# Kernel optimization log

Measured on AMD Instinct MI355X. Metric: run time of the kernel, lower is better.

The kernel has to match this reference:

```python
import jax, jax.numpy as jnp
import numpy as np

SR = 22050
N_SAMPLES = 131072
N_FRAMES = 256
WS = 2048
STEP = WS // 2
C = 32
K = WS // 2 + 1
N_LAYERS = 3
B = 4
SPF = N_SAMPLES // N_FRAMES  # samples per frame = 512


def _morlet(M, w, s):
    # scipy.signal.morlet (complete=True)
    x = np.linspace(-s * 2 * np.pi, s * 2 * np.pi, M)
    return (np.exp(1j * w * x) - np.exp(-0.5 * w ** 2)) * np.exp(-0.5 * x ** 2) * np.pi ** -0.25


def _make_filter_bank():
    # musical_scale_hz(21, 129, K)
    midi = np.linspace(21.0, 129.0, K)
    hz = 440.0 * 2.0 ** ((midi - 69.0) / 12.0)
    basis = np.zeros((K, WS), dtype=np.complex128)
    s = 0.025
    for i, f in enumerate(hz):
        w = f / (s * 2 * SR / WS)
        basis[i] = _morlet(WS, w, s)
    basis = basis.real
    basis = basis / (np.linalg.norm(basis, axis=-1, keepdims=True) + 1e-8)
    # abs(rfft(fb, norm='ortho'))
    spec = np.abs(np.fft.rfft(basis, axis=-1) / np.sqrt(WS))
    return jnp.asarray(spec, dtype=jnp.float32)  # (K, K)


def _hann():
    # torch.hann_window default is periodic
    return 0.5 - 0.5 * jnp.cos(2.0 * jnp.pi * jnp.arange(WS) / WS)


def _windowed_audio(x):
    # pad right by step, unfold into overlapping frames, apply hann window
    xp = jnp.pad(x, ((0, 0), (0, 0), (0, STEP)))
    nf = (xp.shape[-1] - WS) // STEP + 1  # = 128
    idx = jnp.arange(nf)[:, None] * STEP + jnp.arange(WS)[None, :]
    frames = xp[..., idx]  # (B, C, F, WS)
    return frames * _hann()


def _overlap_add(frames):
    # apply_window=True: hann at synthesis, hop = WS//2
    x = frames * _hann()
    b, c, f, w = x.shape
    hop = w // 2
    first = x[..., :hop].reshape(b, c, f * hop)
    second = x[..., hop:].reshape(b, c, f * hop)
    return jnp.pad(first, ((0, 0), (0, 0), (0, hop))) + jnp.pad(second, ((0, 0), (0, 0), (hop, 0)))


def _fft_convolve(a, b):
    n = a.shape[-1]
    pa = [(0, 0)] * (a.ndim - 1) + [(0, n)]
    pb = [(0, 0)] * (b.ndim - 1) + [(0, n)]
    spec = jnp.fft.rfft(jnp.pad(a, pa), axis=-1) * jnp.fft.rfft(jnp.pad(b, pb), axis=-1)
    return jnp.fft.irfft(spec, axis=-1)[..., :n]


def _block(x, transfer, mixer_mat, gain, filter_bank):
    t = x.shape[-1]
    x = jnp.einsum('bct,cd->bdt', x, mixer_mat)  # channel mixing
    frames = _windowed_audio(x)                  # (B, C, F, WS)
    spec = jnp.fft.rfft(frames, axis=-1)         # (B, C, F, K) complex
    T = (transfer @ filter_bank).astype(spec.dtype)  # (C, K)
    spec_f = jnp.moveaxis(spec, 2, 0)            # (F, B, C, K)
    init = jnp.zeros(spec_f.shape[1:], dtype=spec.dtype)

    def step(carry, s):
        out = (s + carry) * T
        return out, out

    _, outs = jax.lax.scan(step, init, spec_f)   # linear recurrence over frames
    out = jnp.moveaxis(outs, 0, 2)               # (B, C, F, K)
    wins = jnp.fft.irfft(out, axis=-1)           # (B, C, F, WS)
    samples = _overlap_add(wins)
    samples = jnp.tanh(samples * gain[None, :, None])
    return samples[..., :t]


def _network(x, transfers, mixer_mats, gains, mixer, filter_bank):
    outputs = [x]
    inp = x
    for i in range(N_LAYERS):
        inp = _block(inp, transfers[i], mixer_mats[i], gains[i], filter_bank)
        outputs.append(inp)
    result = jnp.stack(outputs, axis=-1)         # (B, C, T, L+1)
    w = jax.nn.softmax(mixer)
    mixed = (result * w).sum(-1)                 # mixture over layer outputs
    return mixed.sum(axis=1, keepdims=True)      # (B, 1, T)


def setup_inputs() -> dict:
    key = jax.random.key(0)
    ks = jax.random.split(key, 8)
    sig = jax.random.uniform(ks[0], (B, C, N_FRAMES), dtype=jnp.float32) * 1e-2
    noise = jax.random.uniform(ks[1], (N_SAMPLES,), minval=-1.0, maxval=1.0, dtype=jnp.float32)
    channel_decays = jax.random.uniform(ks[2], (C,), dtype=jnp.float32)
    mixer = jax.random.normal(ks[3], (N_LAYERS + 1,), dtype=jnp.float32)
    res = jax.random.uniform(ks[4], (N_LAYERS, C, K), minval=0.5, maxval=0.9998, dtype=jnp.float32)
    mask = (jax.random.uniform(ks[5], (N_LAYERS, C, K)) < 0.01).astype(jnp.float32)
    transfers = res * mask                       # sparse resonances (p=0.01)
    mixer_mats = jnp.tile(jnp.eye(C, dtype=jnp.float32)[None], (N_LAYERS, 1, 1))
    gains = jax.random.uniform(ks[6], (N_LAYERS, C), minval=1.0, maxval=50.0, dtype=jnp.float32)
    filter_bank = _make_filter_bank()
    return dict(sig=sig, noise=noise, channel_decays=channel_decays, mixer=mixer,
                transfers=transfers, mixer_mats=mixer_mats, gains=gains, filter_bank=filter_bank)


def reference(sig, noise, channel_decays, mixer, transfers, mixer_mats, gains, filter_bank):
    # upsample_with_holes
    us = jnp.zeros((sig.shape[0], C, N_SAMPLES), dtype=sig.dtype).at[..., ::SPF].set(sig)
    # per-channel decaying envelopes
    ls = jnp.linspace(1.0, 0.0, SPF, dtype=sig.dtype)[None, None, :] ** channel_decays[None, :, None]
    ls = jnp.pad(ls, ((0, 0), (0, 0), (0, N_SAMPLES - SPF)))
    us = _fft_convolve(us, ls) * noise
    result = _network(us, transfers, mixer_mats, gains, mixer, filter_bank)
    return result, sig
```

## Files before the change

### kernel.cpp

```cpp
#include <hip/hip_runtime.h>
#include <math.h>

constexpr int BB   = 4;
constexpr int CC   = 32;
constexpr int TT   = 131072;
constexpr int NFRM = 128;
constexpr int KK   = 1025;
constexpr int HOP  = 1024;
constexpr int SPF  = 512;
constexpr int SIGF = 256;
constexpr int NL   = 3;
constexpr int RST  = 2052;
constexpr int NBC  = BB*CC;
constexpr int NROWS = NBC*NFRM;
constexpr int MAXNZ = 256;
constexpr int GRP  = 8;
constexpr int FPG  = 16;

#define PD4(a) ((a) + ((a) >> 3))

__device__ __forceinline__ float4 f4add(float4 a, float4 b){return make_float4(a.x+b.x,a.y+b.y,a.z+b.z,a.w+b.w);}
__device__ __forceinline__ float4 f4sub(float4 a, float4 b){return make_float4(a.x-b.x,a.y-b.y,a.z-b.z,a.w-b.w);}
__device__ __forceinline__ float4 cmul4(float4 v, float c, float s){
  return make_float4(v.x*c - v.y*s, v.x*s + v.y*c, v.z*c - v.w*s, v.z*s + v.w*c);
}

template<int SGN>
__device__ __forceinline__ void dft4p(float4 v[4]) {
  float4 b0=f4add(v[0],v[2]), b1=f4sub(v[0],v[2]), b2=f4add(v[1],v[3]), b3=f4sub(v[1],v[3]);
  float4 ib3 = (SGN<0)? make_float4(b3.y,-b3.x,b3.w,-b3.z) : make_float4(-b3.y,b3.x,-b3.w,b3.z);
  v[0]=f4add(b0,b2); v[2]=f4sub(b0,b2);
  v[1]=f4add(b1,ib3); v[3]=f4sub(b1,ib3);
}

template<int SGN, bool FINAL_STORE>
__device__ __forceinline__ void stockham_pair(float4 v[4], float4* S4, int tid) {
  #pragma unroll
  for (int Ns=1; Ns<1024; Ns*=4) {
    if (Ns>1) {
      int k = tid & (Ns-1);
      float ang = (float)SGN * 6.28318530717958647692f * (float)k / (float)(4*Ns);
      float s1,c1; __sincosf(ang,&s1,&c1);
      float c2=c1*c1-s1*s1, s2=2.f*c1*s1;
      float c3=c2*c1-s2*s1, s3=c2*s1+s2*c1;
      v[1]=cmul4(v[1],c1,s1); v[2]=cmul4(v[2],c2,s2); v[3]=cmul4(v[3],c3,s3);
    }
    dft4p<SGN>(v);
    if (Ns<256 || FINAL_STORE) {
      int idxD = ((tid & ~(Ns-1))<<2) | (tid & (Ns-1));
      S4[PD4(idxD       )] = v[0];
      S4[PD4(idxD +   Ns)] = v[1];
      S4[PD4(idxD + 2*Ns)] = v[2];
      S4[PD4(idxD + 3*Ns)] = v[3];
      __syncthreads();
      if (Ns<256) {
        v[0]=S4[PD4(tid)]; v[1]=S4[PD4(tid+256)]; v[2]=S4[PD4(tid+512)]; v[3]=S4[PD4(tid+768)];
        __syncthreads();
      }
    }
  }
}

__global__ void k_tables(const float* __restrict__ decay, float* __restrict__ ENVt,
                         float* __restrict__ HANN, float* __restrict__ PKt,
                         float* __restrict__ UPKt) {
  int gid = blockIdx.x*256 + threadIdx.x;
  if (gid < CC*SPF) {
    int c = gid >> 9, r = gid & 511;
    float d = decay[c];
    float env;
    if (r == 511) env = (d == 0.f) ? 1.f : 0.f;
    else          env = powf((float)(511-r)*(1.0f/511.0f), d);
    ENVt[gid] = env;
  }
  if (gid < 2048) HANN[gid] = 0.5f - 0.5f*cosf((float)gid*(float)(M_PI/1024.0));
  if (gid <= 1024) { float s,c; sincosf(-(float)M_PI*(float)gid*(1.0f/1024.0f),&s,&c); PKt[2*gid]=c; PKt[2*gid+1]=s; }
  if (gid <  1024) { float s,c; sincosf( (float)M_PI*(float)gid*(1.0f/1024.0f),&s,&c); UPKt[2*gid]=c; UPKt[2*gid+1]=s; }
}

__global__ void __launch_bounds__(64) k_nnz(const float* __restrict__ tr,
    int* __restrict__ NZI, float* __restrict__ NZV, int* __restrict__ NZC) {
  int lc = blockIdx.x;
  int lane = threadIdx.x;
  const float* trow = tr + (size_t)lc*KK;
  int base = 0;
  for (int start = 0; start < KK; start += 64) {
    int kp = start + lane;
    float v = (kp < KK) ? trow[kp] : 0.f;
    unsigned long long m = __ballot(v != 0.f);
    int pos = base + __popcll(m & ((1ull<<lane)-1ull));
    if (v != 0.f && pos < MAXNZ) { NZI[lc*MAXNZ+pos] = kp; NZV[lc*MAXNZ+pos] = v; }
    base += __popcll(m);
  }
  if (lane == 0) NZC[lc] = (base < MAXNZ) ? base : MAXNZ;
}

__global__ void __launch_bounds__(256) k_tmat2(const int* __restrict__ NZI,
    const float* __restrict__ NZV, const int* __restrict__ NZC,
    const float* __restrict__ fb, float* __restrict__ TM) {
  int gid = blockIdx.x*256 + threadIdx.x;
  if (gid >= NL*CC*KK) return;
  int k = gid % KK, lc = gid / KK;
  int n = NZC[lc];
  const int*   zi = NZI + lc*MAXNZ;
  const float* zv = NZV + lc*MAXNZ;
  float acc = 0.f;
  for (int i = 0; i < n; ++i)
    acc = fmaf(zv[i], fb[(size_t)zi[i]*KK + k], acc);
  TM[gid] = acc;
}

__global__ void k_ident(const float* __restrict__ mats, int* __restrict__ FLG) {
  int l = blockIdx.x;
  const float* M = mats + (size_t)l*CC*CC;
  __shared__ int ok;
  if (threadIdx.x == 0) ok = 1;
  __syncthreads();
  for (int i = threadIdx.x; i < CC*CC; i += 256) {
    float ex = ((i>>5) == (i&31)) ? 1.f : 0.f;
    if (M[i] != ex) ok = 0;
  }
  __syncthreads();
  if (threadIdx.x == 0) FLG[l] = ok;
}

__global__ void __launch_bounds__(256) k_us_init(const float* __restrict__ sig,
    const float* __restrict__ noise, const float* __restrict__ mixer,
    const float* __restrict__ M0, const float* __restrict__ ENVt,
    float* __restrict__ X, float* __restrict__ out) {
  __shared__ float sM[CC*CC];
  int tid = threadIdx.x;
  for (int i = tid; i < CC*CC; i += 256) sM[i] = M0[i];
  __syncthreads();
  int gid = blockIdx.x*256 + tid;
  int b = gid >> 17, t = gid & (TT-1);
  int q = t >> 9, r = t & 511;
  float nz = noise[t];
  float u[CC]; float s = 0.f;
  #pragma unroll
  for (int c = 0; c < CC; ++c) { u[c] = sig[(b*CC+c)*SIGF + q] * ENVt[c*SPF + r]; s += u[c]; }
  float m0=mixer[0],m1=mixer[1],m2=mixer[2],m3=mixer[3];
  float mx=fmaxf(fmaxf(m0,m1),fmaxf(m2,m3));
  float e0=__expf(m0-mx),e1=__expf(m1-mx),e2=__expf(m2-mx),e3=__expf(m3-mx);
  float w0=e0/(e0+e1+e2+e3);
  out[gid] = w0 * nz * s;
  #pragma unroll
  for (int d = 0; d < CC; ++d) {
    float acc = 0.f;
    #pragma unroll
    for (int c = 0; c < CC; ++c) acc = fmaf(u[c], sM[c*CC+d], acc);
    X[(size_t)(b*CC+d)*TT + t] = nz * acc;
  }
  if (gid < BB*CC*SIGF) out[BB*TT + gid] = sig[gid];
}

__global__ void __launch_bounds__(256) k_mix_cond(float* __restrict__ X,
    const float* __restrict__ M, const int* __restrict__ FLG, int layer) {
  if (FLG[layer]) return;
  __shared__ float sM[CC*CC];
  int tid = threadIdx.x;
  for (int i = tid; i < CC*CC; i += 256) sM[i] = M[i];
  __syncthreads();
  int gid = blockIdx.x*256 + tid;
  int b = gid >> 17, t = gid & (TT-1);
  float* xp = X + (size_t)b*CC*TT + t;
  float xv[CC];
  #pragma unroll
  for (int c = 0; c < CC; ++c) xv[c] = xp[(size_t)c*TT];
  for (int d = 0; d < CC; ++d) {
    float acc = 0.f;
    #pragma unroll
    for (int c = 0; c < CC; ++c) acc = fmaf(xv[c], sM[c*CC+d], acc);
    xp[(size_t)d*TT] = acc;
  }
}

__global__ void __launch_bounds__(256) k_fwd_scan(const float* __restrict__ X,
    float* __restrict__ SPEC, float* __restrict__ EB, const float* __restrict__ TM,
    const float* __restrict__ HANN, const float* __restrict__ PKt) {
  __shared__ float4 S4[1152];
  int tid = threadIdx.x;
  int blk = blockIdx.x;
  int g = blk & (GRP-1), bc = blk >> 3;
  int c = bc & (CC-1);
  const float* xr = X + (size_t)bc*TT;
  float Tv[5]; float2 cr[5];
  #pragma unroll
  for (int j = 0; j < 5; ++j) {
    int k = tid + 256*j;
    Tv[j] = (k <= 1024) ? TM[c*KK + k] : 0.f;
    cr[j] = make_float2(0.f, 0.f);
  }
  for (int p = 0; p < 8; ++p) {
    int f0 = g*FPG + 2*p;
    int s0 = f0*HOP;
    float4 v[4];
    #pragma unroll
    for (int r = 0; r < 4; ++r) {
      int n = tid + 256*r;
      float2 h = *(const float2*)(HANN + 2*n);
      float2 a = *(const float2*)(xr + s0 + 2*n);
      int sb = s0 + HOP + 2*n;
      float2 bb = (sb < TT) ? *(const float2*)(xr + sb) : make_float2(0.f,0.f);
      v[r] = make_float4(a.x*h.x, a.y*h.y, bb.x*h.x, bb.y*h.y);
    }
    stockham_pair<-1, true>(v, S4, tid);
    float* row0 = SPEC + (size_t)(bc*NFRM + f0)*RST;
    float* row1 = row0 + RST;
    #pragma unroll
    for (int j = 0; j < 5; ++j) {
      int k = tid + 256*j;
      if (k <= 1024) {
        float4 Zk = S4[PD4(k & 1023)];
        float4 Zm = S4[PD4((1024-k) & 1023)];
        float2 pk = *(const float2*)(PKt + 2*k);
        float zex = 0.5f*(Zk.x+Zm.x), zey = 0.5f*(Zk.y-Zm.y);
        float zox = 0.5f*(Zk.y+Zm.y), zoy = -0.5f*(Zk.x-Zm.x);
        float sax = zex + pk.x*zox - pk.y*zoy;
        float say = zey + pk.x*zoy + pk.y*zox;
        zex = 0.5f*(Zk.z+Zm.z); zey = 0.5f*(Zk.w-Zm.w);
        zox = 0.5f*(Zk.w+Zm.w); zoy = -0.5f*(Zk.z-Zm.z);
        float sbx = zex + pk.x*zox - pk.y*zoy;
        float sby = zey + pk.x*zoy + pk.y*zox;
        cr[j].x = (sax + cr[j].x)*Tv[j];
        cr[j].y = (say + cr[j].y)*Tv[j];
        *(float2*)(row0 + 2*k) = cr[j];
        cr[j].x = (sbx + cr[j].x)*Tv[j];
        cr[j].y = (sby + cr[j].y)*Tv[j];
        *(float2*)(row1 + 2*k) = cr[j];
      }
    }
    __syncthreads();
  }
  float* er = EB + (size_t)blk*RST;
  #pragma unroll
  for (int j = 0; j < 5; ++j) {
    int k = tid + 256*j;
    if (k <= 1024) *(float2*)(er + 2*k) = cr[j];
  }
}

__global__ void __launch_bounds__(256) k_carry(float* __restrict__ EB, const float* __restrict__ TM) {
  int gid = blockIdx.x*256 + threadIdx.x;
  if (gid >= NBC*KK) return;
  int bc = gid / KK, k = gid - bc*KK;
  int c = bc & (CC-1);
  float T = TM[c*KK + k];
  float t2 = T*T, t4 = t2*t2, t8 = t4*t4, T16 = t8*t8;
  float2 cc = make_float2(0.f, 0.f);
  for (int g = 0; g < GRP; ++g) {
    float* p = EB + (size_t)(bc*GRP + g)*RST + 2*k;
    float2 e = *(float2*)p;
    *(float2*)p = cc;
    cc.x = e.x + T16*cc.x;
    cc.y = e.y + T16*cc.y;
  }
}

__global__ void __launch_bounds__(256) k_inv_ola(const float* __restrict__ SPEC,
    const float* __restrict__ EB, const float* __restrict__ TM,
    const float* __restrict__ HANN, const float* __restrict__ UPKt,
    const float* __restrict__ gains, float* __restrict__ X) {
  __shared__ float4 S4[1152];
  int tid = threadIdx.x;
  int blk = blockIdx.x;
  int g = blk & (GRP-1), bc = blk >> 3;
  int c = bc & (CC-1);
  int fb = g*FPG;
  float sg = gains[c];
  const float* ec = EB + (size_t)blk*RST;
  float Tn[4], Tm[4], facn[4], facm[4];
  float2 cinN[4], cinM[4];
  #pragma unroll
  for (int r = 0; r < 4; ++r) {
    int n = tid + 256*r, m = 1024 - n;
    Tn[r] = TM[c*KK + n]; Tm[r] = TM[c*KK + m];
    facn[r] = Tn[r]; facm[r] = Tm[r];
    cinN[r] = *(const float2*)(ec + 2*n);
    cinM[r] = *(const float2*)(ec + 2*m);
  }
  float2 pr0 = make_float2(0.f,0.f), pr1 = make_float2(0.f,0.f);
  float* xw = X + (size_t)bc*TT;
  const float sc = 1.0f/1024.0f;
  for (int rnd = 0; rnd < 9; ++rnd) {
    float4 v[4];
    #pragma unroll
    for (int r = 0; r < 4; ++r) {
      int n = tid + 256*r, m = 1024 - n;
      float2 An, Am, Bn, Bm;
      if (rnd == 0) { An = cinN[r]; Am = cinM[r]; }
      else {
        const float* rowA = SPEC + (size_t)(bc*NFRM + fb + 2*rnd - 1)*RST;
        float2 a = *(const float2*)(rowA + 2*n);
        float2 b = *(const float2*)(rowA + 2*m);
        An = make_float2(a.x + facn[r]*cinN[r].x, a.y + facn[r]*cinN[r].y);
        Am = make_float2(b.x + facm[r]*cinM[r].x, b.y + facm[r]*cinM[r].y);
        facn[r] *= Tn[r]; facm[r] *= Tm[r];
      }
      if (rnd < 8) {
        const float* rowB = SPEC + (size_t)(bc*NFRM + fb + 2*rnd)*RST;
        float2 a = *(const float2*)(rowB + 2*n);
        float2 b = *(const float2*)(rowB + 2*m);
        Bn = make_float2(a.x + facn[r]*cinN[r].x, a.y + facn[r]*cinN[r].y);
        Bm = make_float2(b.x + facm[r]*cinM[r].x, b.y + facm[r]*cinM[r].y);
        facn[r] *= Tn[r]; facm[r] *= Tm[r];
      } else { Bn = make_float2(0.f,0.f); Bm = make_float2(0.f,0.f); }
      float2 u = *(const float2*)(UPKt + 2*n);
      float zex = 0.5f*(An.x+Am.x), zey = 0.5f*(An.y-Am.y);
      float dx  = 0.5f*(An.x-Am.x), dy  = 0.5f*(An.y+Am.y);
      float zox = u.x*dx - u.y*dy, zoy = u.x*dy + u.y*dx;
      v[r].x = zex - zoy; v[r].y = zey + zox;
      zex = 0.5f*(Bn.x+Bm.x); zey = 0.5f*(Bn.y-Bm.y);
      dx  = 0.5f*(Bn.x-Bm.x); dy  = 0.5f*(Bn.y+Bm.y);
      zox = u.x*dx - u.y*dy; zoy = u.x*dy + u.y*dx;
      v[r].z = zex - zoy; v[r].w = zey + zox;
    }
    stockham_pair<1, false>(v, S4, tid);
    #pragma unroll
    for (int r = 0; r < 4; ++r) {
      int n = tid + 256*r;
      float2 h = *(const float2*)(HANN + 2*n);
      v[r].x *= sc*h.x; v[r].y *= sc*h.y;
      v[r].z *= sc*h.x; v[r].w *= sc*h.y;
    }
    if (rnd >= 1) {
      int tbase = (fb + 2*rnd - 1)*HOP;
      float2 o0 = make_float2(tanhf(sg*(v[0].x + pr0.x)), tanhf(sg*(v[0].y + pr0.y)));
      float2 o1 = make_float2(tanhf(sg*(v[1].x + pr1.x)), tanhf(sg*(v[1].y + pr1.y)));
      *(float2*)(xw + tbase + 2*tid)        = o0;
      *(float2*)(xw + tbase + 2*(tid+256))  = o1;
    }
    if (rnd < 8) {
      int tbase = (fb + 2*rnd)*HOP;
      float2 o0 = make_float2(tanhf(sg*(v[0].z + v[2].x)), tanhf(sg*(v[0].w + v[2].y)));
      float2 o1 = make_float2(tanhf(sg*(v[1].z + v[3].x)), tanhf(sg*(v[1].w + v[3].y)));
      *(float2*)(xw + tbase + 2*tid)        = o0;
      *(float2*)(xw + tbase + 2*(tid+256))  = o1;
      pr0 = make_float2(v[2].z, v[2].w);
      pr1 = make_float2(v[3].z, v[3].w);
    }
  }
}

__global__ void __launch_bounds__(256) k_out(const float* __restrict__ X,
    const float* __restrict__ mixer, int layer, float* __restrict__ out) {
  int gid = blockIdx.x*256 + threadIdx.x;
  int t4 = gid*4;
  int b = t4 >> 17, t = t4 & (TT-1);
  float m0=mixer[0],m1=mixer[1],m2=mixer[2],m3=mixer[3];
  float mx=fmaxf(fmaxf(m0,m1),fmaxf(m2,m3));
  float e[4]={__expf(m0-mx),__expf(m1-mx),__expf(m2-mx),__expf(m3-mx)};
  float w = e[layer+1]/(e[0]+e[1]+e[2]+e[3]);
  float4 acc = make_float4(0.f,0.f,0.f,0.f);
  #pragma unroll
  for (int c = 0; c < CC; ++c) {
    float4 xv = *(const float4*)(X + (size_t)(b*CC+c)*TT + t);
    acc.x += xv.x; acc.y += xv.y; acc.z += xv.z; acc.w += xv.w;
  }
  float4 o = *(float4*)(out + t4);
  o.x += w*acc.x; o.y += w*acc.y; o.z += w*acc.z; o.w += w*acc.w;
  *(float4*)(out + t4) = o;
}

extern "C" void kernel_launch(void* const* d_in, const int* in_sizes, int n_in,
                              void* d_out, int out_size, void* d_ws, size_t ws_size,
                              hipStream_t stream) {
  const float* sig        = (const float*)d_in[0];
  const float* noise      = (const float*)d_in[1];
  const float* decay      = (const float*)d_in[2];
  const float* mixer      = (const float*)d_in[3];
  const float* transfers  = (const float*)d_in[4];
  const float* mixer_mats = (const float*)d_in[5];
  const float* gains      = (const float*)d_in[6];
  const float* fb         = (const float*)d_in[7];
  float* out = (float*)d_out;
  float* ws  = (float*)d_ws;

  float* X    = ws;
  float* SPEC = X + (size_t)16777216;
  float* EB   = SPEC + (size_t)NROWS*RST;
  float* TM   = EB + (size_t)NBC*GRP*RST;
  float* ENVt = TM + (size_t)NL*CC*KK;
  float* HANN = ENVt + CC*SPF;
  float* PKt  = HANN + 2048;
  float* UPKt = PKt + 2050;
  float* NZVf = UPKt + 2048;
  int*   NZI  = (int*)(NZVf + NL*CC*MAXNZ);
  int*   NZC  = NZI + NL*CC*MAXNZ;
  int*   FLG  = NZC + NL*CC;

  k_tables<<<64, 256, 0, stream>>>(decay, ENVt, HANN, PKt, UPKt);
  k_nnz<<<NL*CC, 64, 0, stream>>>(transfers, NZI, NZVf, NZC);
  k_tmat2<<<(NL*CC*KK + 255)/256, 256, 0, stream>>>(NZI, NZVf, NZC, fb, TM);
  k_ident<<<NL, 256, 0, stream>>>(mixer_mats, FLG);
  k_us_init<<<BB*TT/256, 256, 0, stream>>>(sig, noise, mixer, mixer_mats, ENVt, X, out);

  for (int l = 0; l < NL; ++l) {
    const float* TMl = TM + (size_t)l*CC*KK;
    if (l > 0)
      k_mix_cond<<<BB*TT/256, 256, 0, stream>>>(X, mixer_mats + (size_t)l*CC*CC, FLG, l);
    k_fwd_scan<<<NBC*GRP, 256, 0, stream>>>(X, SPEC, EB, TMl, HANN, PKt);
    k_carry<<<(NBC*KK + 255)/256, 256, 0, stream>>>(EB, TMl);
    k_inv_ola<<<NBC*GRP, 256, 0, stream>>>(SPEC, EB, TMl, HANN, UPKt, gains + (size_t)l*CC, X);
    k_out<<<BB*TT/1024, 256, 0, stream>>>(X, mixer, l, out);
  }
}
```

Baseline: 532.1 us.

## Double frame groups per channel and stage inverse spectrum rows through LDS

Splits each channel's 128 frames into 16 groups of 8 instead of 8 groups of 16, doubling the number of blocks in the forward scan and inverse/OLA kernels, and adjusts the carry recurrence to use T^8. The inverse kernel now loads each spectrum row once with coalesced reads into shared memory, then reads the mirrored n and 1024-n bins from LDS, instead of issuing two scattered global loads per bin. This aims at more parallelism and fewer redundant global reads. In exchange it adds two block barriers per round, an extra pass of overlap rounds per group, and more carry-buffer traffic.

```diff
diff --git a/kernel.cpp b/kernel.cpp
--- a/kernel.cpp
+++ b/kernel.cpp
@@ -14,8 +14,8 @@
 constexpr int NBC  = BB*CC;
 constexpr int NROWS = NBC*NFRM;
 constexpr int MAXNZ = 256;
-constexpr int GRP  = 8;
-constexpr int FPG  = 16;
+constexpr int GRP  = 16;
+constexpr int FPG  = 8;
 
 #define PD4(a) ((a) + ((a) >> 3))
 
@@ -181,7 +181,7 @@
   __shared__ float4 S4[1152];
   int tid = threadIdx.x;
   int blk = blockIdx.x;
-  int g = blk & (GRP-1), bc = blk >> 3;
+  int g = blk & (GRP-1), bc = blk >> 4;
   int c = bc & (CC-1);
   const float* xr = X + (size_t)bc*TT;
   float Tv[5]; float2 cr[5];
@@ -191,7 +191,7 @@
     Tv[j] = (k <= 1024) ? TM[c*KK + k] : 0.f;
     cr[j] = make_float2(0.f, 0.f);
   }
-  for (int p = 0; p < 8; ++p) {
+  for (int p = 0; p < FPG/2; ++p) {
     int f0 = g*FPG + 2*p;
     int s0 = f0*HOP;
     float4 v[4];
@@ -246,14 +246,14 @@
   int bc = gid / KK, k = gid - bc*KK;
   int c = bc & (CC-1);
   float T = TM[c*KK + k];
-  float t2 = T*T, t4 = t2*t2, t8 = t4*t4, T16 = t8*t8;
+  float t2 = T*T, t4 = t2*t2, T8 = t4*t4;
   float2 cc = make_float2(0.f, 0.f);
   for (int g = 0; g < GRP; ++g) {
     float* p = EB + (size_t)(bc*GRP + g)*RST + 2*k;
     float2 e = *(float2*)p;
     *(float2*)p = cc;
-    cc.x = e.x + T16*cc.x;
-    cc.y = e.y + T16*cc.y;
+    cc.x = e.x + T8*cc.x;
+    cc.y = e.y + T8*cc.y;
   }
 }
 
@@ -262,49 +262,52 @@
     const float* __restrict__ HANN, const float* __restrict__ UPKt,
     const float* __restrict__ gains, float* __restrict__ X) {
   __shared__ float4 S4[1152];
+  float2* XSA = (float2*)S4;
+  float2* XSB = XSA + 1026;
   int tid = threadIdx.x;
   int blk = blockIdx.x;
-  int g = blk & (GRP-1), bc = blk >> 3;
+  int g = blk & (GRP-1), bc = blk >> 4;
   int c = bc & (CC-1);
   int fb = g*FPG;
   float sg = gains[c];
   const float* ec = EB + (size_t)blk*RST;
-  float Tn[4], Tm[4], facn[4], facm[4];
-  float2 cinN[4], cinM[4];
-  #pragma unroll
-  for (int r = 0; r < 4; ++r) {
-    int n = tid + 256*r, m = 1024 - n;
-    Tn[r] = TM[c*KK + n]; Tm[r] = TM[c*KK + m];
-    facn[r] = Tn[r]; facm[r] = Tm[r];
-    cinN[r] = *(const float2*)(ec + 2*n);
-    cinM[r] = *(const float2*)(ec + 2*m);
+  float tv[5], cu[5]; float2 cr[5];
+  #pragma unroll
+  for (int j = 0; j < 5; ++j) {
+    int k = tid + 256*j;
+    tv[j] = (k <= 1024) ? TM[c*KK + k] : 0.f;
+    cr[j] = (k <= 1024) ? *(const float2*)(ec + 2*k) : make_float2(0.f,0.f);
+    cu[j] = 1.f;
   }
   float2 pr0 = make_float2(0.f,0.f), pr1 = make_float2(0.f,0.f);
   float* xw = X + (size_t)bc*TT;
   const float sc = 1.0f/1024.0f;
-  for (int rnd = 0; rnd < 9; ++rnd) {
+  for (int rnd = 0; rnd < FPG/2 + 1; ++rnd) {
+    const float* rowA = SPEC + (size_t)(bc*NFRM + fb + 2*rnd - 1)*RST;
+    const float* rowB = rowA + RST;
+    #pragma unroll
+    for (int j = 0; j < 5; ++j) {
+      int k = tid + 256*j;
+      if (k <= 1024) {
+        float facA = cu[j], facB = cu[j]*tv[j];
+        float2 a;
+        if (rnd == 0) a = cr[j];
+        else { float2 s = *(const float2*)(rowA + 2*k);
+               a = make_float2(s.x + facA*cr[j].x, s.y + facA*cr[j].y); }
+        XSA[k] = a;
+        float2 b = make_float2(0.f,0.f);
+        if (rnd < FPG/2) { float2 s = *(const float2*)(rowB + 2*k);
+               b = make_float2(s.x + facB*cr[j].x, s.y + facB*cr[j].y); }
+        XSB[k] = b;
+        cu[j] = facB*tv[j];
+      }
+    }
+    __syncthreads();
     float4 v[4];
     #pragma unroll
     for (int r = 0; r < 4; ++r) {
       int n = tid + 256*r, m = 1024 - n;
-      float2 An, Am, Bn, Bm;
-      if (rnd == 0) { An = cinN[r]; Am = cinM[r]; }
-      else {
-        const float* rowA = SPEC + (size_t)(bc*NFRM + fb + 2*rnd - 1)*RST;
-        float2 a = *(const float2*)(rowA + 2*n);
-        float2 b = *(const float2*)(rowA + 2*m);
-        An = make_float2(a.x + facn[r]*cinN[r].x, a.y + facn[r]*cinN[r].y);
-        Am = make_float2(b.x + facm[r]*cinM[r].x, b.y + facm[r]*cinM[r].y);
-        facn[r] *= Tn[r]; facm[r] *= Tm[r];
-      }
-      if (rnd < 8) {
-        const float* rowB = SPEC + (size_t)(bc*NFRM + fb + 2*rnd)*RST;
-        float2 a = *(const float2*)(rowB + 2*n);
-        float2 b = *(const float2*)(rowB + 2*m);
-        Bn = make_float2(a.x + facn[r]*cinN[r].x, a.y + facn[r]*cinN[r].y);
-        Bm = make_float2(b.x + facm[r]*cinM[r].x, b.y + facm[r]*cinM[r].y);
-        facn[r] *= Tn[r]; facm[r] *= Tm[r];
-      } else { Bn = make_float2(0.f,0.f); Bm = make_float2(0.f,0.f); }
+      float2 An = XSA[n], Am = XSA[m], Bn = XSB[n], Bm = XSB[m];
       float2 u = *(const float2*)(UPKt + 2*n);
       float zex = 0.5f*(An.x+Am.x), zey = 0.5f*(An.y-Am.y);
       float dx  = 0.5f*(An.x-Am.x), dy  = 0.5f*(An.y+Am.y);
@@ -315,6 +318,7 @@
       zox = u.x*dx - u.y*dy; zoy = u.x*dy + u.y*dx;
       v[r].z = zex - zoy; v[r].w = zey + zox;
     }
+    __syncthreads();
     stockham_pair<1, false>(v, S4, tid);
     #pragma unroll
     for (int r = 0; r < 4; ++r) {
@@ -330,7 +334,7 @@
       *(float2*)(xw + tbase + 2*tid)        = o0;
       *(float2*)(xw + tbase + 2*(tid+256))  = o1;
     }
-    if (rnd < 8) {
+    if (rnd < FPG/2) {
       int tbase = (fb + 2*rnd)*HOP;
       float2 o0 = make_float2(tanhf(sg*(v[0].z + v[2].x)), tanhf(sg*(v[0].w + v[2].y)));
       float2 o1 = make_float2(tanhf(sg*(v[1].z + v[3].x)), tanhf(sg*(v[1].w + v[3].y)));
```

After: 583.4 us. 1.1x slower.

## Fuse channel-sum output into inverse OLA via atomics, skip final-layer X write

Applied to the files above, without the earlier changes.

Removes the separate k_out kernel, which re-read all 32 channels of X to add a weighted channel sum into the output. Each inverse/OLA block now atomically adds its weighted tanh outputs straight into the output buffer. On the last layer it also skips writing X. The trade is a large number of float atomics contending across the 32 channels per batch, plus non-deterministic summation order; the carry recurrence is also rewritten to decay the carry in place.

```diff
diff --git a/kernel.cpp b/kernel.cpp
--- a/kernel.cpp
+++ b/kernel.cpp
@@ -191,7 +191,7 @@
     Tv[j] = (k <= 1024) ? TM[c*KK + k] : 0.f;
     cr[j] = make_float2(0.f, 0.f);
   }
-  for (int p = 0; p < 8; ++p) {
+  for (int p = 0; p < FPG/2; ++p) {
     int f0 = g*FPG + 2*p;
     int s0 = f0*HOP;
     float4 v[4];
@@ -260,50 +260,57 @@
 __global__ void __launch_bounds__(256) k_inv_ola(const float* __restrict__ SPEC,
     const float* __restrict__ EB, const float* __restrict__ TM,
     const float* __restrict__ HANN, const float* __restrict__ UPKt,
-    const float* __restrict__ gains, float* __restrict__ X) {
+    const float* __restrict__ gains, const float* __restrict__ mixer, int layer,
+    int writeX, float* __restrict__ X, float* __restrict__ out) {
   __shared__ float4 S4[1152];
   int tid = threadIdx.x;
   int blk = blockIdx.x;
   int g = blk & (GRP-1), bc = blk >> 3;
   int c = bc & (CC-1);
+  int b = bc / CC;
   int fb = g*FPG;
   float sg = gains[c];
+  float m0=mixer[0],m1=mixer[1],m2=mixer[2],m3=mixer[3];
+  float mx=fmaxf(fmaxf(m0,m1),fmaxf(m2,m3));
+  float e0=__expf(m0-mx),e1=__expf(m1-mx),e2=__expf(m2-mx),e3=__expf(m3-mx);
+  float ww = ((layer==0)?e1:(layer==1)?e2:e3) / (e0+e1+e2+e3);
   const float* ec = EB + (size_t)blk*RST;
-  float Tn[4], Tm[4], facn[4], facm[4];
-  float2 cinN[4], cinM[4];
+  float Tn[4], Tm[4]; float2 dN[4], dM[4];
   #pragma unroll
   for (int r = 0; r < 4; ++r) {
     int n = tid + 256*r, m = 1024 - n;
     Tn[r] = TM[c*KK + n]; Tm[r] = TM[c*KK + m];
-    facn[r] = Tn[r]; facm[r] = Tm[r];
-    cinN[r] = *(const float2*)(ec + 2*n);
-    cinM[r] = *(const float2*)(ec + 2*m);
+    dN[r] = *(const float2*)(ec + 2*n);
+    dM[r] = *(const float2*)(ec + 2*m);
   }
   float2 pr0 = make_float2(0.f,0.f), pr1 = make_float2(0.f,0.f);
   float* xw = X + (size_t)bc*TT;
+  float* ob = out + (size_t)b*TT;
   const float sc = 1.0f/1024.0f;
-  for (int rnd = 0; rnd < 9; ++rnd) {
+  for (int rnd = 0; rnd < FPG/2 + 1; ++rnd) {
     float4 v[4];
     #pragma unroll
     for (int r = 0; r < 4; ++r) {
       int n = tid + 256*r, m = 1024 - n;
       float2 An, Am, Bn, Bm;
-      if (rnd == 0) { An = cinN[r]; Am = cinM[r]; }
+      if (rnd == 0) { An = dN[r]; Am = dM[r]; }
       else {
         const float* rowA = SPEC + (size_t)(bc*NFRM + fb + 2*rnd - 1)*RST;
         float2 a = *(const float2*)(rowA + 2*n);
-        float2 b = *(const float2*)(rowA + 2*m);
-        An = make_float2(a.x + facn[r]*cinN[r].x, a.y + facn[r]*cinN[r].y);
-        Am = make_float2(b.x + facm[r]*cinM[r].x, b.y + facm[r]*cinM[r].y);
-        facn[r] *= Tn[r]; facm[r] *= Tm[r];
+        float2 bv = *(const float2*)(rowA + 2*m);
+        dN[r].x *= Tn[r]; dN[r].y *= Tn[r];
+        dM[r].x *= Tm[r]; dM[r].y *= Tm[r];
+        An = make_float2(a.x + dN[r].x, a.y + dN[r].y);
+        Am = make_float2(bv.x + dM[r].x, bv.y + dM[r].y);
       }
-      if (rnd < 8) {
+      if (rnd < FPG/2) {
         const float* rowB = SPEC + (size_t)(bc*NFRM + fb + 2*rnd)*RST;
         float2 a = *(const float2*)(rowB + 2*n);
-        float2 b = *(const float2*)(rowB + 2*m);
-        Bn = make_float2(a.x + facn[r]*cinN[r].x, a.y + facn[r]*cinN[r].y);
-        Bm = make_float2(b.x + facm[r]*cinM[r].x, b.y + facm[r]*cinM[r].y);
-        facn[r] *= Tn[r]; facm[r] *= Tm[r];
+        float2 bv = *(const float2*)(rowB + 2*m);
+        dN[r].x *= Tn[r]; dN[r].y *= Tn[r];
+        dM[r].x *= Tm[r]; dM[r].y *= Tm[r];
+        Bn = make_float2(a.x + dN[r].x, a.y + dN[r].y);
+        Bm = make_float2(bv.x + dM[r].x, bv.y + dM[r].y);
       } else { Bn = make_float2(0.f,0.f); Bm = make_float2(0.f,0.f); }
       float2 u = *(const float2*)(UPKt + 2*n);
       float zex = 0.5f*(An.x+Am.x), zey = 0.5f*(An.y-Am.y);
@@ -327,39 +334,31 @@
       int tbase = (fb + 2*rnd - 1)*HOP;
       float2 o0 = make_float2(tanhf(sg*(v[0].x + pr0.x)), tanhf(sg*(v[0].y + pr0.y)));
       float2 o1 = make_float2(tanhf(sg*(v[1].x + pr1.x)), tanhf(sg*(v[1].y + pr1.y)));
-      *(float2*)(xw + tbase + 2*tid)        = o0;
-      *(float2*)(xw + tbase + 2*(tid+256))  = o1;
-    }
-    if (rnd < 8) {
+      if (writeX) {
+        *(float2*)(xw + tbase + 2*tid)        = o0;
+        *(float2*)(xw + tbase + 2*(tid+256))  = o1;
+      }
+      atomicAdd(ob + tbase + 2*tid,       ww*o0.x);
+      atomicAdd(ob + tbase + 2*tid + 1,   ww*o0.y);
+      atomicAdd(ob + tbase + 2*(tid+256),     ww*o1.x);
+      atomicAdd(ob + tbase + 2*(tid+256) + 1, ww*o1.y);
+    }
+    if (rnd < FPG/2) {
       int tbase = (fb + 2*rnd)*HOP;
       float2 o0 = make_float2(tanhf(sg*(v[0].z + v[2].x)), tanhf(sg*(v[0].w + v[2].y)));
       float2 o1 = make_float2(tanhf(sg*(v[1].z + v[3].x)), tanhf(sg*(v[1].w + v[3].y)));
-      *(float2*)(xw + tbase + 2*tid)        = o0;
-      *(float2*)(xw + tbase + 2*(tid+256))  = o1;
+      if (writeX) {
+        *(float2*)(xw + tbase + 2*tid)        = o0;
+        *(float2*)(xw + tbase + 2*(tid+256))  = o1;
+      }
+      atomicAdd(ob + tbase + 2*tid,       ww*o0.x);
+      atomicAdd(ob + tbase + 2*tid + 1,   ww*o0.y);
+      atomicAdd(ob + tbase + 2*(tid+256),     ww*o1.x);
+      atomicAdd(ob + tbase + 2*(tid+256) + 1, ww*o1.y);
       pr0 = make_float2(v[2].z, v[2].w);
       pr1 = make_float2(v[3].z, v[3].w);
     }
   }
-}
-
-__global__ void __launch_bounds__(256) k_out(const float* __restrict__ X,
-    const float* __restrict__ mixer, int layer, float* __restrict__ out) {
-  int gid = blockIdx.x*256 + threadIdx.x;
-  int t4 = gid*4;
-  int b = t4 >> 17, t = t4 & (TT-1);
-  float m0=mixer[0],m1=mixer[1],m2=mixer[2],m3=mixer[3];
-  float mx=fmaxf(fmaxf(m0,m1),fmaxf(m2,m3));
-  float e[4]={__expf(m0-mx),__expf(m1-mx),__expf(m2-mx),__expf(m3-mx)};
-  float w = e[layer+1]/(e[0]+e[1]+e[2]+e[3]);
-  float4 acc = make_float4(0.f,0.f,0.f,0.f);
-  #pragma unroll
-  for (int c = 0; c < CC; ++c) {
-    float4 xv = *(const float4*)(X + (size_t)(b*CC+c)*TT + t);
-    acc.x += xv.x; acc.y += xv.y; acc.z += xv.z; acc.w += xv.w;
-  }
-  float4 o = *(float4*)(out + t4);
-  o.x += w*acc.x; o.y += w*acc.y; o.z += w*acc.z; o.w += w*acc.w;
-  *(float4*)(out + t4) = o;
 }
 
 extern "C" void kernel_launch(void* const* d_in, const int* in_sizes, int n_in,
@@ -401,7 +400,8 @@
       k_mix_cond<<<BB*TT/256, 256, 0, stream>>>(X, mixer_mats + (size_t)l*CC*CC, FLG, l);
     k_fwd_scan<<<NBC*GRP, 256, 0, stream>>>(X, SPEC, EB, TMl, HANN, PKt);
     k_carry<<<(NBC*KK + 255)/256, 256, 0, stream>>>(EB, TMl);
-    k_inv_ola<<<NBC*GRP, 256, 0, stream>>>(SPEC, EB, TMl, HANN, UPKt, gains + (size_t)l*CC, X);
-    k_out<<<BB*TT/1024, 256, 0, stream>>>(X, mixer, l, out);
-  }
-}
+    k_inv_ola<<<NBC*GRP, 256, 0, stream>>>(SPEC, EB, TMl, HANN, UPKt,
+                                           gains + (size_t)l*CC, mixer, l,
+                                           (l < NL-1) ? 1 : 0, X, out);
+  }
+}
```

After: 775.4 us. +45.7%, slower.
